# Kernel tuning notes

Hardware: AMD Instinct MI355X
Metric: run time of the kernel (lower is better)

Reference implementation:

```python
import jax, jax.numpy as jnp
import numpy as np

B, C, L = 32, 128, 4096
TIME_DIM = 512
K_TOP = 8


def setup_inputs() -> dict:
    key = jax.random.key(0)
    k1, k2, k3, k4 = jax.random.split(key, 4)
    x = jax.random.normal(k1, (B, C, L), dtype=jnp.float32)
    time_emb = jax.random.normal(k2, (B, TIME_DIM), dtype=jnp.float32)
    # nn.Linear(time_dim, channels): weight (C, time_dim), bias (C,)
    W = jax.random.normal(k3, (C, TIME_DIM), dtype=jnp.float32) / np.sqrt(TIME_DIM)
    b = jax.random.normal(k4, (C,), dtype=jnp.float32) * 0.01
    return {"x": x, "time_emb": time_emb, "W": W, "b": b}


def reference(x, time_emb, W, b):
    Bn, Cn, n = x.shape
    k = min(K_TOP, n // 2 + 1)
    # time-conditioned modulation: Linear -> tanh -> (1 + tanh) scale
    scale = time_emb @ W.T + b                      # (B, C)
    x_mod = x * (1.0 + jnp.tanh(scale))[:, :, None]  # (B, C, L)
    # rFFT along time
    x_fft = jnp.fft.rfft(x_mod, axis=-1)             # (B, C, F) complex64
    amp = jnp.abs(x_fft)
    # top-k frequency bins per (b, c) row
    _, topk_idx = jax.lax.top_k(amp, k)              # (B, C, k)
    gathered = jnp.take_along_axis(x_fft, topk_idx, axis=-1)
    bi = jnp.arange(Bn)[:, None, None]
    ci = jnp.arange(Cn)[None, :, None]
    masked_fft = jnp.zeros_like(x_fft).at[bi, ci, topk_idx].set(gathered)
    p_it = jnp.fft.irfft(masked_fft, n=n, axis=-1)
    return p_it.astype(x.dtype)
```

## Files before the change

### kernel.cpp

```cpp
#include <hip/hip_runtime.h>

#define LL 4096
#define THREADS 512
#define KK 8

typedef float v2f __attribute__((ext_vector_type(2)));

#define PD(i) ((i) + ((i) >> 4))
#define PERM8(r) ((((r) & 3) << 1) | ((r) >> 2))

__device__ __forceinline__ float sinr(float x) {
    float r; asm("v_sin_f32 %0, %1" : "=v"(r) : "v"(x)); return r;
}
__device__ __forceinline__ float cosr(float x) {
    float r; asm("v_cos_f32 %0, %1" : "=v"(r) : "v"(x)); return r;
}

__device__ __forceinline__ v2f padd(v2f a, v2f b) {
    v2f d; asm("v_pk_add_f32 %0, %1, %2" : "=v"(d) : "v"(a), "v"(b)); return d;
}
__device__ __forceinline__ v2f psub(v2f a, v2f b) {
    v2f d; asm("v_pk_add_f32 %0, %1, %2 neg_lo:[0,1] neg_hi:[0,1]" : "=v"(d) : "v"(a), "v"(b)); return d;
}
__device__ __forceinline__ v2f pmul(v2f a, v2f b) {
    v2f d; asm("v_pk_mul_f32 %0, %1, %2" : "=v"(d) : "v"(a), "v"(b)); return d;
}
__device__ __forceinline__ v2f addmi(v2f a, v2f b) {
    v2f d; asm("v_pk_add_f32 %0, %1, %2 op_sel:[0,1] op_sel_hi:[1,0] neg_hi:[0,1]" : "=v"(d) : "v"(a), "v"(b)); return d;
}
__device__ __forceinline__ v2f submi(v2f a, v2f b) {
    v2f d; asm("v_pk_add_f32 %0, %1, %2 op_sel:[0,1] op_sel_hi:[1,0] neg_lo:[0,1]" : "=v"(d) : "v"(a), "v"(b)); return d;
}
__device__ __forceinline__ v2f negi(v2f a) {
    v2f d; asm("v_pk_add_f32 %0, %1, 0 op_sel:[1,0] op_sel_hi:[0,0] neg_hi:[1,0]" : "=v"(d) : "v"(a)); return d;
}
__device__ __forceinline__ v2f pfma(v2f a, v2f b, v2f c) {
    v2f d; asm("v_pk_fma_f32 %0, %1, %2, %3" : "=v"(d) : "v"(a), "v"(b), "v"(c)); return d;
}
__device__ __forceinline__ v2f pfms(v2f a, v2f b, v2f c) {
    v2f d; asm("v_pk_fma_f32 %0, %1, %2, %3 neg_lo:[0,0,1] neg_hi:[0,0,1]" : "=v"(d) : "v"(a), "v"(b), "v"(c)); return d;
}
__device__ __forceinline__ v2f cmul(v2f a, v2f b) {
    v2f t, d;
    asm("v_pk_mul_f32 %0, %1, %2 op_sel:[0,0] op_sel_hi:[0,1]" : "=v"(t) : "v"(a), "v"(b));
    asm("v_pk_fma_f32 %0, %1, %2, %3 op_sel:[1,1,0] op_sel_hi:[1,0,1] neg_lo:[1,0,0]"
        : "=v"(d) : "v"(a), "v"(b), "v"(t));
    return d;
}
__device__ __forceinline__ v2f cmulw(v2f z, v2f w) {
    v2f t, d;
    asm("v_pk_mul_f32 %0, %1, %2 op_sel:[0,0] op_sel_hi:[1,0]" : "=v"(t) : "v"(z), "v"(w));
    asm("v_pk_fma_f32 %0, %1, %2, %3 op_sel:[1,1,0] op_sel_hi:[0,1,1] neg_hi:[1,0,0]"
        : "=v"(d) : "v"(z), "v"(w), "v"(t));
    return d;
}
__device__ __forceinline__ v2f unt0(v2f z, v2f y) {
    v2f d; asm("v_pk_add_f32 %0, %1, %2 neg_hi:[0,1]" : "=v"(d) : "v"(z), "v"(y)); return d;
}
__device__ __forceinline__ v2f unt1(v2f z, v2f y) {
    v2f d; asm("v_pk_add_f32 %0, %1, %2 op_sel:[1,1] op_sel_hi:[0,0] neg_hi:[1,0]" : "=v"(d) : "v"(z), "v"(y)); return d;
}

__device__ __forceinline__ void dft4(v2f& a, v2f& b, v2f& c, v2f& d) {
    v2f t0 = padd(a, c), t1 = psub(a, c);
    v2f t2 = padd(b, d), t3 = psub(b, d);
    a = padd(t0, t2); c = psub(t0, t2);
    b = addmi(t1, t3); d = submi(t1, t3);
}

__device__ __forceinline__ void dft8(v2f* v) {
    dft4(v[0], v[2], v[4], v[6]);
    dft4(v[1], v[3], v[5], v[7]);
    const float C2 = 0.70710678118654752f;
    const v2f W81 = (v2f){C2, C2};
    const v2f W83 = (v2f){-C2, C2};
    v[3] = cmulw(v[3], W81);
    v[5] = negi(v[5]);
    v[7] = cmulw(v[7], W83);
#pragma unroll
    for (int k0 = 0; k0 < 4; ++k0) {
        v2f a = v[2 * k0], b = v[2 * k0 + 1];
        v[2 * k0]     = padd(a, b);
        v[2 * k0 + 1] = psub(a, b);
    }
}

__device__ __forceinline__ void twiddle7w(v2f* v, v2f w1) {
    v2f w2 = cmul(w1, w1);
    v2f w3 = cmul(w2, w1);
    v2f w4 = cmul(w2, w2);
    v2f w5 = cmul(w3, w2);
    v2f w6 = cmul(w3, w3);
    v2f w7 = cmul(w4, w3);
    v[1] = cmulw(v[1], w1);
    v[2] = cmulw(v[2], w2);
    v[3] = cmulw(v[3], w3);
    v[4] = cmulw(v[4], w4);
    v[5] = cmulw(v[5], w5);
    v[6] = cmulw(v[6], w6);
    v[7] = cmulw(v[7], w7);
}

#define DPP_STEP(CTRL)                                                          \
  {                                                                             \
    int vs_ = __builtin_amdgcn_update_dpp(__float_as_int(bv), __float_as_int(bv), \
                                          CTRL, 0xf, 0xf, false);               \
    int bs_ = __builtin_amdgcn_update_dpp(bb, bb, CTRL, 0xf, 0xf, false);       \
    float vf_ = __int_as_float(vs_);                                            \
    bool tk_ = (vf_ > bv) || (vf_ == bv && bs_ < bb);                           \
    bv = tk_ ? vf_ : bv; bb = tk_ ? bs_ : bb;                                   \
  }
#define DPP_ADD(CTRL)                                                           \
  ps += __int_as_float(__builtin_amdgcn_update_dpp(0, __float_as_int(ps),       \
                                                   CTRL, 0xf, 0xf, true));

__global__ __launch_bounds__(THREADS, 8)
void fft2_topk_k(const float* __restrict__ x, const float* __restrict__ te,
                 const float* __restrict__ W, const float* __restrict__ bias,
                 float* __restrict__ out) {
    __shared__ v2f zb[4353];
    __shared__ float wv[8];
    __shared__ float candV[2][16];
    __shared__ int   candB[2][16];
    __shared__ v2f  selAB[2][KK];
    __shared__ int  selF[2][KK];
    __shared__ v2f  T1[64], T2[64];

    int t = threadIdx.x;
    int pair = blockIdx.x;
    int b = pair >> 6;
    int c0 = (pair & 63) << 1;
    int row0 = (b << 7) + c0;

    const float* xp0 = x + (size_t)row0 * LL;
    const float* xp1 = xp0 + LL;
    v2f v[8];
#pragma unroll
    for (int r = 0; r < 8; ++r) { v[r].x = xp0[t + 512 * r]; v[r].y = xp1[t + 512 * r]; }

    {
        int mh = t >> 8, tt = t & 255;
        const float* tp = te + b * 512;
        const float* wp = W + (c0 + mh) * 512;
        float ps = tp[tt] * wp[tt] + tp[tt + 256] * wp[tt + 256];
        DPP_ADD(0x111) DPP_ADD(0x112) DPP_ADD(0x114) DPP_ADD(0x118)
        DPP_ADD(0x142) DPP_ADD(0x143)
        if ((t & 63) == 63) wv[t >> 6] = ps;
    }
    if (t < 64) {
        float a = (float)t * (1.0f / 64.0f);
        T1[t] = (v2f){cosr(a), sinr(a)};
    } else if (t < 128) {
        float a = (float)(t - 64) * (1.0f / 4096.0f);
        T2[t - 64] = (v2f){cosr(a), sinr(a)};
    }

    dft8(v);
    {
        int wb = 8 * t + (t >> 1);
#pragma unroll
        for (int r = 0; r < 8; ++r) zb[wb + r] = v[PERM8(r)];
    }
    __syncthreads();

    int rb = t + (t >> 4);

    {
        v2f w1 = T1[t & 7];
#pragma unroll
        for (int r = 0; r < 8; ++r) v[r] = zb[rb + 544 * r];
        twiddle7w(v, w1);
    }
    dft8(v);
    __syncthreads();
    {
        int wb = 64 * (t >> 3) + (t & 7);
        int B0 = wb + (wb >> 4);
        int B1 = (wb + 8) + ((wb + 8) >> 4);
#pragma unroll
        for (int s = 0; s < 4; ++s) {
            zb[B0 + 17 * s] = v[PERM8(2 * s)];
            zb[B1 + 17 * s] = v[PERM8(2 * s + 1)];
        }
    }
    __syncthreads();

    {
        v2f w1 = cmul(T1[(t & 63) >> 3], T2[(t & 7) << 3]);
#pragma unroll
        for (int r = 0; r < 8; ++r) v[r] = zb[rb + 544 * r];
        twiddle7w(v, w1);
    }
    dft8(v);
    __syncthreads();
    {
        int wb = 512 * (t >> 6) + (t & 63);
        int B2 = wb + (wb >> 4);
#pragma unroll
        for (int r = 0; r < 8; ++r) zb[B2 + 68 * r] = v[PERM8(r)];
    }
    __syncthreads();

    {
        v2f w1 = cmul(T1[t >> 6], T2[t & 63]);
#pragma unroll
        for (int r = 0; r < 8; ++r) v[r] = zb[rb + 544 * r];
        twiddle7w(v, w1);
    }
    dft8(v);
#pragma unroll
    for (int r = 0; r < 8; ++r) zb[rb + 544 * r] = v[PERM8(r)];
    if (t == 0) zb[4352] = v[0];
    __syncthreads();

    int wid = t >> 6, lane = t & 63;

    if (wid < 4) {
        int row = wid >> 1, hf = wid & 1;
        int kb = (hf << 10) + lane;
        int base1 = PD(kb);
        int base2 = PD(4096 - kb);
        float amp[16];
        float lv = -1.f; int lm = 0;
#pragma unroll
        for (int m = 0; m < 16; ++m) {
            v2f z = zb[base1 + 68 * m];
            v2f y = zb[base2 - 68 * m];
            v2f X = row ? unt1(z, y) : unt0(z, y);
            float a = fmaf(X.x, X.x, X.y * X.y);
            amp[m] = a;
            if (a > lv) { lv = a; lm = m; }
        }
        for (int it = 0; it < KK; ++it) {
            float bv = lv; int bb = kb + (lm << 6);
            DPP_STEP(0x111)
            DPP_STEP(0x112)
            DPP_STEP(0x114)
            DPP_STEP(0x118)
            DPP_STEP(0x142)
            DPP_STEP(0x143)
            float vwin = __int_as_float(__builtin_amdgcn_readlane(__float_as_int(bv), 63));
            int   wbin = __builtin_amdgcn_readlane(bb, 63);
            if (lane == 0) { candV[row][(hf << 3) + it] = vwin; candB[row][(hf << 3) + it] = wbin; }
            if ((wbin & 63) == lane) {
                int m0 = ((wbin - (hf << 10)) >> 6);
                lv = -1.f; lm = 0;
#pragma unroll
                for (int m = 0; m < 16; ++m) {
                    float a = (m == m0) ? -1.f : amp[m];
                    amp[m] = a;
                    if (a > lv) { lv = a; lm = m; }
                }
            }
        }
    }
    __syncthreads();

    if (wid < 2 && lane < 17) {
        int row = wid;
        float g = 1.0f + tanhf(wv[4 * row] + wv[4 * row + 1] + wv[4 * row + 2]
                               + wv[4 * row + 3] + bias[c0 + row]);
        v2f z2 = zb[PD(2048)];
        float xn = 2.f * (row ? z2.y : z2.x);
        float a2048 = xn * xn;
        float myv; int myb, rank;
        if (lane < 16) {
            myv = candV[row][lane]; myb = candB[row][lane];
            rank = lane & 7;
            int ob = (lane < 8) ? 8 : 0;
#pragma unroll
            for (int j = 0; j < 8; ++j) {
                float ov = candV[row][ob + j]; int obn = candB[row][ob + j];
                if (ov > myv || (ov == myv && obn < myb)) rank++;
            }
            if (a2048 > myv) rank++;
        } else {
            myv = a2048; myb = 2048; rank = 0;
#pragma unroll
            for (int j = 0; j < 16; ++j)
                if (candV[row][j] >= myv) rank++;
        }
        if (rank < KK) {
            v2f z = zb[PD(myb)];
            v2f y = zb[PD(4096 - myb)];
            v2f X;
            if (row == 0) X = (v2f){0.5f * (z.x + y.x), 0.5f * (z.y - y.y)};
            else          X = (v2f){0.5f * (z.y + y.y), 0.5f * (y.x - z.x)};
            bool edge = (myb == 0) || (myb == 2048);
            float wgt = (edge ? 1.f : 2.f) * g * (1.0f / 4096.0f);
            selF[row][rank] = myb;
            selAB[row][rank] = (v2f){wgt * X.x, edge ? 0.f : wgt * X.y};
        }
    }
    __syncthreads();

    {
        int mh = t >> 8, u = t & 255;
        v2f rc[4], rp[4], tcv[4], sgv[4];
#pragma unroll
        for (int j = 0; j < 4; ++j) {
            int f0 = selF[mh][2 * j], f1 = selF[mh][2 * j + 1];
            v2f A0 = selAB[mh][2 * j], A1 = selAB[mh][2 * j + 1];
            int m0 = (f0 * u) & 4095, m1 = (f1 * u) & 4095;
            v2f e0 = cmul(T1[m0 >> 6], T2[m0 & 63]);
            v2f e1 = cmul(T1[m1 >> 6], T2[m1 & 63]);
            v2f w0 = cmul(A0, e0);
            v2f w1 = cmul(A1, e1);
            v2f s0 = T1[(f0 & 15) << 2];
            v2f s1 = T1[(f1 & 15) << 2];
            rc[j] = (v2f){w0.x, w1.x};
            rp[j] = (v2f){w0.x * s0.x + w0.y * s0.y, w1.x * s1.x + w1.y * s1.y};
            tcv[j] = (v2f){s0.x + s0.x, s1.x + s1.x};
            sgv[j] = (v2f){(f0 & 1) ? -1.f : 1.f, (f1 & 1) ? -1.f : 1.f};
        }
        float* op = out + (size_t)(row0 + mh) * LL;
#pragma unroll
        for (int q2 = 0; q2 < 8; ++q2) {
            v2f accv = padd(padd(rc[0], rc[1]), padd(rc[2], rc[3]));
            v2f acdv = pfma(rc[0], sgv[0],
                       pfma(rc[1], sgv[1],
                       pfma(rc[2], sgv[2], pmul(rc[3], sgv[3]))));
            op[u + (q2 << 8)] = accv.x + accv.y;
            op[u + (q2 << 8) + 2048] = acdv.x + acdv.y;
#pragma unroll
            for (int j = 0; j < 4; ++j) {
                v2f rn = pfms(tcv[j], rc[j], rp[j]);
                rp[j] = rc[j];
                rc[j] = rn;
            }
        }
    }
}

extern "C" void kernel_launch(void* const* d_in, const int* in_sizes, int n_in,
                              void* d_out, int out_size, void* d_ws, size_t ws_size,
                              hipStream_t stream) {
    const float* x    = (const float*)d_in[0];
    const float* te   = (const float*)d_in[1];
    const float* W    = (const float*)d_in[2];
    const float* bias = (const float*)d_in[3];
    float* out = (float*)d_out;
    fft2_topk_k<<<2048, THREADS, 0, stream>>>(x, te, W, bias, out);
}
```

Before: 46.84 us.

## Use half-length complex FFT per row instead of packing two rows

Switches from computing two real rows as one complex 4096-point FFT to the standard real-FFT trick: each row is packed as even/odd samples into a 2048-point complex FFT, and the spectrum is recovered with a twiddle post-processing step. Blocks now handle one row with 256 threads and the grid doubles to 4096, halving shared memory per block. The last radix stage becomes radix-4 with fused twiddles, and the top-k search plus ranking run across four waves with 32 candidates. This cuts FFT work and LDS footprint per block, in exchange for extra twiddle math during unpacking and a larger rank-merge step.

```diff
diff --git a/kernel.cpp b/kernel.cpp
--- a/kernel.cpp
+++ b/kernel.cpp
@@ -1,7 +1,6 @@
 #include <hip/hip_runtime.h>
 
-#define LL 4096
-#define THREADS 512
+#define THREADS 256
 #define KK 8
 
 typedef float v2f __attribute__((ext_vector_type(2)));
@@ -33,6 +32,9 @@
 }
 __device__ __forceinline__ v2f negi(v2f a) {
     v2f d; asm("v_pk_add_f32 %0, %1, 0 op_sel:[1,0] op_sel_hi:[0,0] neg_hi:[1,0]" : "=v"(d) : "v"(a)); return d;
+}
+__device__ __forceinline__ v2f posi(v2f a) {
+    v2f d; asm("v_pk_add_f32 %0, %1, 0 op_sel:[1,0] op_sel_hi:[0,0] neg_lo:[1,0]" : "=v"(d) : "v"(a)); return d;
 }
 __device__ __forceinline__ v2f pfma(v2f a, v2f b, v2f c) {
     v2f d; asm("v_pk_fma_f32 %0, %1, %2, %3" : "=v"(d) : "v"(a), "v"(b), "v"(c)); return d;
@@ -72,11 +74,9 @@
     dft4(v[0], v[2], v[4], v[6]);
     dft4(v[1], v[3], v[5], v[7]);
     const float C2 = 0.70710678118654752f;
-    const v2f W81 = (v2f){C2, C2};
-    const v2f W83 = (v2f){-C2, C2};
-    v[3] = cmulw(v[3], W81);
+    v[3] = cmulw(v[3], (v2f){C2, C2});
     v[5] = negi(v[5]);
-    v[7] = cmulw(v[7], W83);
+    v[7] = cmulw(v[7], (v2f){-C2, C2});
 #pragma unroll
     for (int k0 = 0; k0 < 4; ++k0) {
         v2f a = v[2 * k0], b = v[2 * k0 + 1];
@@ -115,34 +115,30 @@
                                                    CTRL, 0xf, 0xf, true));
 
 __global__ __launch_bounds__(THREADS, 8)
-void fft2_topk_k(const float* __restrict__ x, const float* __restrict__ te,
+void fft1_topk_k(const float* __restrict__ x, const float* __restrict__ te,
                  const float* __restrict__ W, const float* __restrict__ bias,
                  float* __restrict__ out) {
-    __shared__ v2f zb[4353];
-    __shared__ float wv[8];
-    __shared__ float candV[2][16];
-    __shared__ int   candB[2][16];
-    __shared__ v2f  selAB[2][KK];
-    __shared__ int  selF[2][KK];
+    __shared__ v2f zb[2177];
+    __shared__ float wv[4];
+    __shared__ float candV[32];
+    __shared__ int   candB[32];
+    __shared__ v2f  selAB[KK];
+    __shared__ int  selF[KK];
     __shared__ v2f  T1[64], T2[64];
 
     int t = threadIdx.x;
-    int pair = blockIdx.x;
-    int b = pair >> 6;
-    int c0 = (pair & 63) << 1;
-    int row0 = (b << 7) + c0;
-
-    const float* xp0 = x + (size_t)row0 * LL;
-    const float* xp1 = xp0 + LL;
+    int row = blockIdx.x;
+    int b = row >> 7, c = row & 127;
+
+    const v2f* xp = (const v2f*)(x + (size_t)row * 4096);
     v2f v[8];
 #pragma unroll
-    for (int r = 0; r < 8; ++r) { v[r].x = xp0[t + 512 * r]; v[r].y = xp1[t + 512 * r]; }
-
-    {
-        int mh = t >> 8, tt = t & 255;
+    for (int r = 0; r < 8; ++r) v[r] = xp[t + 256 * r];
+
+    {
         const float* tp = te + b * 512;
-        const float* wp = W + (c0 + mh) * 512;
-        float ps = tp[tt] * wp[tt] + tp[tt + 256] * wp[tt + 256];
+        const float* wp = W + c * 512;
+        float ps = tp[t] * wp[t] + tp[t + 256] * wp[t + 256];
         DPP_ADD(0x111) DPP_ADD(0x112) DPP_ADD(0x114) DPP_ADD(0x118)
         DPP_ADD(0x142) DPP_ADD(0x143)
         if ((t & 63) == 63) wv[t >> 6] = ps;
@@ -165,12 +161,9 @@
 
     int rb = t + (t >> 4);
 
-    {
-        v2f w1 = T1[t & 7];
-#pragma unroll
-        for (int r = 0; r < 8; ++r) v[r] = zb[rb + 544 * r];
-        twiddle7w(v, w1);
-    }
+#pragma unroll
+    for (int r = 0; r < 8; ++r) v[r] = zb[rb + 272 * r];
+    twiddle7w(v, T1[t & 7]);
     dft8(v);
     __syncthreads();
     {
@@ -185,12 +178,9 @@
     }
     __syncthreads();
 
-    {
-        v2f w1 = cmul(T1[(t & 63) >> 3], T2[(t & 7) << 3]);
-#pragma unroll
-        for (int r = 0; r < 8; ++r) v[r] = zb[rb + 544 * r];
-        twiddle7w(v, w1);
-    }
+#pragma unroll
+    for (int r = 0; r < 8; ++r) v[r] = zb[rb + 272 * r];
+    twiddle7w(v, cmul(T1[(t & 63) >> 3], T2[(t & 7) << 3]));
     dft8(v);
     __syncthreads();
     {
@@ -201,52 +191,57 @@
     }
     __syncthreads();
 
-    {
-        v2f w1 = cmul(T1[t >> 6], T2[t & 63]);
-#pragma unroll
-        for (int r = 0; r < 8; ++r) v[r] = zb[rb + 544 * r];
-        twiddle7w(v, w1);
-    }
-    dft8(v);
-#pragma unroll
-    for (int r = 0; r < 8; ++r) zb[rb + 544 * r] = v[PERM8(r)];
-    if (t == 0) zb[4352] = v[0];
+#pragma unroll
+    for (int s = 0; s < 8; ++s) v[s] = zb[rb + 272 * s];
+    {
+        const float C2 = 0.70710678118654752f;
+        v2f wA  = cmul(T1[(2 * t) >> 6], T2[(2 * t) & 63]);
+        v2f wA2 = cmul(wA, wA);
+        v2f wA3 = cmul(wA2, wA);
+        v2f wB  = cmul(wA, (v2f){C2, C2});
+        v2f wB2 = posi(wA2);
+        v2f wB3 = cmul(wA3, (v2f){-C2, C2});
+        v[2] = cmulw(v[2], wA);  v[4] = cmulw(v[4], wA2); v[6] = cmulw(v[6], wA3);
+        v[3] = cmulw(v[3], wB);  v[5] = cmulw(v[5], wB2); v[7] = cmulw(v[7], wB3);
+        dft4(v[0], v[2], v[4], v[6]);
+        dft4(v[1], v[3], v[5], v[7]);
+    }
+#pragma unroll
+    for (int s = 0; s < 8; ++s) zb[rb + 272 * s] = v[s];
+    if (t == 0) zb[2176] = v[0];
     __syncthreads();
 
     int wid = t >> 6, lane = t & 63;
 
-    if (wid < 4) {
-        int row = wid >> 1, hf = wid & 1;
-        int kb = (hf << 10) + lane;
+    {
+        int kb = (wid << 9) + lane;
         int base1 = PD(kb);
-        int base2 = PD(4096 - kb);
-        float amp[16];
+        int base2 = PD(2048 - kb);
+        v2f tl2 = T2[lane];
+        float amp[8];
         float lv = -1.f; int lm = 0;
 #pragma unroll
-        for (int m = 0; m < 16; ++m) {
+        for (int m = 0; m < 8; ++m) {
             v2f z = zb[base1 + 68 * m];
             v2f y = zb[base2 - 68 * m];
-            v2f X = row ? unt1(z, y) : unt0(z, y);
-            float a = fmaf(X.x, X.x, X.y * X.y);
+            v2f wtw = cmul(T1[8 * wid + m], tl2);
+            v2f Xp = padd(unt0(z, y), cmulw(unt1(z, y), wtw));
+            float a = fmaf(Xp.x, Xp.x, Xp.y * Xp.y);
             amp[m] = a;
             if (a > lv) { lv = a; lm = m; }
         }
         for (int it = 0; it < KK; ++it) {
             float bv = lv; int bb = kb + (lm << 6);
-            DPP_STEP(0x111)
-            DPP_STEP(0x112)
-            DPP_STEP(0x114)
-            DPP_STEP(0x118)
-            DPP_STEP(0x142)
-            DPP_STEP(0x143)
+            DPP_STEP(0x111) DPP_STEP(0x112) DPP_STEP(0x114)
+            DPP_STEP(0x118) DPP_STEP(0x142) DPP_STEP(0x143)
             float vwin = __int_as_float(__builtin_amdgcn_readlane(__float_as_int(bv), 63));
             int   wbin = __builtin_amdgcn_readlane(bb, 63);
-            if (lane == 0) { candV[row][(hf << 3) + it] = vwin; candB[row][(hf << 3) + it] = wbin; }
+            if (lane == 0) { candV[(wid << 3) + it] = vwin; candB[(wid << 3) + it] = wbin; }
             if ((wbin & 63) == lane) {
-                int m0 = ((wbin - (hf << 10)) >> 6);
+                int m0 = ((wbin - (wid << 9)) >> 6);
                 lv = -1.f; lm = 0;
 #pragma unroll
-                for (int m = 0; m < 16; ++m) {
+                for (int m = 0; m < 8; ++m) {
                     float a = (m == m0) ? -1.f : amp[m];
                     amp[m] = a;
                     if (a > lv) { lv = a; lm = m; }
@@ -256,52 +251,52 @@
     }
     __syncthreads();
 
-    if (wid < 2 && lane < 17) {
-        int row = wid;
-        float g = 1.0f + tanhf(wv[4 * row] + wv[4 * row + 1] + wv[4 * row + 2]
-                               + wv[4 * row + 3] + bias[c0 + row]);
-        v2f z2 = zb[PD(2048)];
-        float xn = 2.f * (row ? z2.y : z2.x);
+    if (wid == 0 && lane < 33) {
+        float g = 1.0f + tanhf(wv[0] + wv[1] + wv[2] + wv[3] + bias[c]);
+        v2f z0 = zb[0];
+        float xn = 2.f * (z0.x - z0.y);
         float a2048 = xn * xn;
         float myv; int myb, rank;
-        if (lane < 16) {
-            myv = candV[row][lane]; myb = candB[row][lane];
-            rank = lane & 7;
-            int ob = (lane < 8) ? 8 : 0;
-#pragma unroll
-            for (int j = 0; j < 8; ++j) {
-                float ov = candV[row][ob + j]; int obn = candB[row][ob + j];
+        if (lane < 32) {
+            myv = candV[lane]; myb = candB[lane];
+            rank = 0;
+#pragma unroll
+            for (int j = 0; j < 32; ++j) {
+                float ov = candV[j]; int obn = candB[j];
                 if (ov > myv || (ov == myv && obn < myb)) rank++;
             }
             if (a2048 > myv) rank++;
         } else {
             myv = a2048; myb = 2048; rank = 0;
 #pragma unroll
-            for (int j = 0; j < 16; ++j)
-                if (candV[row][j] >= myv) rank++;
+            for (int j = 0; j < 32; ++j)
+                if (candV[j] >= myv) rank++;
         }
         if (rank < KK) {
-            v2f z = zb[PD(myb)];
-            v2f y = zb[PD(4096 - myb)];
-            v2f X;
-            if (row == 0) X = (v2f){0.5f * (z.x + y.x), 0.5f * (z.y - y.y)};
-            else          X = (v2f){0.5f * (z.y + y.y), 0.5f * (y.x - z.x)};
+            float Xr, Xi;
+            if (myb == 2048) { Xr = xn; Xi = 0.f; }
+            else {
+                v2f z = zb[PD(myb)];
+                v2f y = zb[PD(2048 - myb)];
+                v2f wtw = cmul(T1[myb >> 6], T2[myb & 63]);
+                v2f Xp = padd(unt0(z, y), cmulw(unt1(z, y), wtw));
+                Xr = Xp.x; Xi = Xp.y;
+            }
             bool edge = (myb == 0) || (myb == 2048);
-            float wgt = (edge ? 1.f : 2.f) * g * (1.0f / 4096.0f);
-            selF[row][rank] = myb;
-            selAB[row][rank] = (v2f){wgt * X.x, edge ? 0.f : wgt * X.y};
-        }
-    }
-    __syncthreads();
-
-    {
-        int mh = t >> 8, u = t & 255;
+            float wgt = (edge ? 1.f : 2.f) * g * (0.5f / 4096.0f);
+            selF[rank] = myb;
+            selAB[rank] = (v2f){wgt * Xr, edge ? 0.f : wgt * Xi};
+        }
+    }
+    __syncthreads();
+
+    {
         v2f rc[4], rp[4], tcv[4], sgv[4];
 #pragma unroll
         for (int j = 0; j < 4; ++j) {
-            int f0 = selF[mh][2 * j], f1 = selF[mh][2 * j + 1];
-            v2f A0 = selAB[mh][2 * j], A1 = selAB[mh][2 * j + 1];
-            int m0 = (f0 * u) & 4095, m1 = (f1 * u) & 4095;
+            int f0 = selF[2 * j], f1 = selF[2 * j + 1];
+            v2f A0 = selAB[2 * j], A1 = selAB[2 * j + 1];
+            int m0 = (f0 * t) & 4095, m1 = (f1 * t) & 4095;
             v2f e0 = cmul(T1[m0 >> 6], T2[m0 & 63]);
             v2f e1 = cmul(T1[m1 >> 6], T2[m1 & 63]);
             v2f w0 = cmul(A0, e0);
@@ -313,15 +308,15 @@
             tcv[j] = (v2f){s0.x + s0.x, s1.x + s1.x};
             sgv[j] = (v2f){(f0 & 1) ? -1.f : 1.f, (f1 & 1) ? -1.f : 1.f};
         }
-        float* op = out + (size_t)(row0 + mh) * LL;
-#pragma unroll
-        for (int q2 = 0; q2 < 8; ++q2) {
+        float* op = out + (size_t)row * 4096;
+#pragma unroll
+        for (int q = 0; q < 8; ++q) {
             v2f accv = padd(padd(rc[0], rc[1]), padd(rc[2], rc[3]));
             v2f acdv = pfma(rc[0], sgv[0],
                        pfma(rc[1], sgv[1],
                        pfma(rc[2], sgv[2], pmul(rc[3], sgv[3]))));
-            op[u + (q2 << 8)] = accv.x + accv.y;
-            op[u + (q2 << 8) + 2048] = acdv.x + acdv.y;
+            op[t + (q << 8)] = accv.x + accv.y;
+            op[t + (q << 8) + 2048] = acdv.x + acdv.y;
 #pragma unroll
             for (int j = 0; j < 4; ++j) {
                 v2f rn = pfms(tcv[j], rc[j], rp[j]);
@@ -340,5 +335,5 @@
     const float* W    = (const float*)d_in[2];
     const float* bias = (const float*)d_in[3];
     float* out = (float*)d_out;
-    fft2_topk_k<<<2048, THREADS, 0, stream>>>(x, te, W, bias, out);
-}
+    fft1_topk_k<<<4096, THREADS, 0, stream>>>(x, te, W, bias, out);
+}
```

New measurement: 52.49 us. 12.1% more time.
